# Optimization experiments

Hardware: AMD Instinct MI355X
Metric: run time of the kernel (lower is better)

## Reference

```python
import jax, jax.numpy as jnp
import numpy as np

H, D, G = 8, 64, 64          # num_heads, head_dim, num_slices
HID = H * D                  # 512
EPS = 1e-5
N = 100000


def setup_inputs() -> dict:
    key = jax.random.key(0)
    ks = jax.random.split(key, 16)
    s = 0.02  # init scale
    return {
        "x": jax.random.normal(ks[0], (N, HID), dtype=jnp.float32),
        # x_proj / fx_proj: Linear(HID -> HID) with bias, eqx stores W as (out, in)
        "Wx": jax.random.normal(ks[1], (HID, HID), dtype=jnp.float32) * s,
        "bx": jax.random.normal(ks[2], (HID,), dtype=jnp.float32) * s,
        "Wfx": jax.random.normal(ks[3], (HID, HID), dtype=jnp.float32) * s,
        "bfx": jax.random.normal(ks[4], (HID,), dtype=jnp.float32) * s,
        # slice_proj: Linear(D -> G) with bias
        "Ws": jax.random.normal(ks[5], (G, D), dtype=jnp.float32) * s,
        "bs": jax.random.normal(ks[6], (G,), dtype=jnp.float32) * s,
        # learned temperature, init 0.5, shape (H,1,1)
        "temperature": jnp.ones((H, 1, 1), dtype=jnp.float32) * 0.5,
        # slice MultiheadAttention (num_heads=1, size D): q/k/v/out proj, no biases (eqx defaults)
        "Wq": jax.random.normal(ks[7], (D, D), dtype=jnp.float32) * s,
        "Wk": jax.random.normal(ks[8], (D, D), dtype=jnp.float32) * s,
        "Wv": jax.random.normal(ks[9], (D, D), dtype=jnp.float32) * s,
        "Wo": jax.random.normal(ks[10], (D, D), dtype=jnp.float32) * s,
        # out_proj: Linear(HID -> HID) with bias
        "Wout": jax.random.normal(ks[11], (HID, HID), dtype=jnp.float32) * s,
        "bout": jax.random.normal(ks[12], (HID,), dtype=jnp.float32) * s,
    }


def reference(x, Wx, bx, Wfx, bfx, Ws, bs, temperature, Wq, Wk, Wv, Wo, Wout, bout):
    n = x.shape[0]
    # token projections, split into heads: (H, N, D)
    x_mid = (x @ Wx.T + bx).reshape(n, H, D).transpose(1, 0, 2)
    fx_mid = (x @ Wfx.T + bfx).reshape(n, H, D).transpose(1, 0, 2)

    # slice weights: proj -> temperature-scaled softmax over G  (H, N, G)
    logits = jnp.einsum('hnd,gd->hng', x_mid, Ws) + bs
    w = jax.nn.softmax(logits * temperature, axis=-1)

    # weighted pooling to slice tokens (H, G, D)
    norm = w.sum(axis=1)                                   # (H, G)
    tokens = jnp.einsum('hnd,hng->hgd', fx_mid, w) / (norm[..., None] + EPS)

    # small single-head attention over the G slice tokens, vmapped over H
    q = jnp.einsum('hgd,od->hgo', tokens, Wq)
    k = jnp.einsum('hgd,od->hgo', tokens, Wk)
    v = jnp.einsum('hgd,od->hgo', tokens, Wv)
    attn = jax.nn.softmax(jnp.einsum('hgd,hkd->hgk', q, k) / jnp.sqrt(jnp.float32(D)), axis=-1)
    out_tok = jnp.einsum('hgk,hkd->hgd', attn, v)
    out_tok = jnp.einsum('hgd,od->hgo', out_tok, Wo)

    # deslice: weighted unpooling back to tokens, merge heads, output projection
    out = jnp.einsum('hgd,hng->hnd', out_tok, w)           # (H, N, D)
    out = out.transpose(1, 0, 2).reshape(n, HID)
    return out @ Wout.T + bout
```

## Files before the change

kernel.cpp:

```cpp
#include <hip/hip_runtime.h>
#include <hip/hip_bf16.h>

#define HID 512
#define NH  8
#define DD  64
#define GG  64
#define EPSF 1e-5f

typedef __attribute__((ext_vector_type(8))) short short8;
typedef __attribute__((ext_vector_type(4))) short short4v;
typedef __attribute__((ext_vector_type(4))) float floatx4;

__device__ __forceinline__ short f2bf(float f) {
    union { float f; unsigned u; } v; v.f = f;
    unsigned r = v.u + 0x7fffu + ((v.u >> 16) & 1u);
    return (short)(r >> 16);
}
__device__ __forceinline__ float bf2f(short s) {
    union { unsigned u; float f; } v;
    v.u = ((unsigned)(unsigned short)s) << 16;
    return v.f;
}

#define GLOAD_LDS16(g, l) __builtin_amdgcn_global_load_lds( \
    (const __attribute__((address_space(1))) unsigned int*)(g), \
    (__attribute__((address_space(3))) unsigned int*)(l), 16, 0, 0)

__global__ __launch_bounds__(256)
void cast_kernel(const float* __restrict__ x, short* __restrict__ xb, int n8) {
    int i = blockIdx.x * 256 + threadIdx.x;
    if (i >= n8) return;
    const float4* p = (const float4*)(x + (size_t)i * 8);
    float4 a = p[0], b = p[1];
    short8 v;
    v[0] = f2bf(a.x); v[1] = f2bf(a.y); v[2] = f2bf(a.z); v[3] = f2bf(a.w);
    v[4] = f2bf(b.x); v[5] = f2bf(b.y); v[6] = f2bf(b.z); v[7] = f2bf(b.w);
    *(short8*)(xb + (size_t)i * 8) = v;
}

__global__ void fold1_kernel(const float* __restrict__ Wx, const float* __restrict__ bx,
                             const float* __restrict__ Wfx, const float* __restrict__ bfx,
                             const float* __restrict__ Ws, const float* __restrict__ bs,
                             const float* __restrict__ temp,
                             short* __restrict__ Wcat, float* __restrict__ bias_cat) {
    int idx = blockIdx.x * 256 + threadIdx.x;
    int row = idx >> 9;
    int k = idx & 511;
    float val;
    if (row < 512) {
        val = Wfx[row * 512 + k];
        if (k == 0) bias_cat[row] = bfx[row];
    } else {
        int hg = row - 512;
        int h = hg >> 6, g = hg & 63;
        float t = temp[h];
        float s = 0.f;
        #pragma unroll 8
        for (int d = 0; d < 64; ++d) s += Ws[g * 64 + d] * Wx[(h * 64 + d) * 512 + k];
        val = s * t;
        if (k == 0) {
            float b = 0.f;
            for (int d = 0; d < 64; ++d) b += Ws[g * 64 + d] * bx[h * 64 + d];
            bias_cat[row] = (b + bs[g]) * t;
        }
    }
    Wcat[idx] = f2bf(val);
}

template <bool OUT_F32, bool FUSE_SM>
__global__ __launch_bounds__(256, 4)
void gemm_bt(const short* __restrict__ A, int lda,
             const short* __restrict__ B,
             const float* __restrict__ bias,
             void* __restrict__ Cp, int ldc,
             int M, int K, int clog2, int Rtiles) {
    __shared__ short As[128 * 64];
    __shared__ short Bs[128 * 64];

    const int id = blockIdx.x;
    const int xcd = id & 7;
    const int s = id >> 3;
    const int cblk = s & ((1 << clog2) - 1);
    const int slice = (Rtiles + 7) >> 3;
    const int rt = xcd * slice + (s >> clog2);
    if (rt >= Rtiles) return;

    const int tid = threadIdx.x;
    const int wid = tid >> 6, lane = tid & 63;
    const int col0 = cblk * 128;
    const int row0 = rt * 128;
    const int wm = (wid >> 1) * 64, wn = (wid & 1) * 64;
    const int lr = lane & 15, lq = lane >> 4;

    int st_row[4], st_kc[4];
    #pragma unroll
    for (int it = 0; it < 4; ++it) {
        int c = tid + it * 256;
        st_row[it] = c >> 3;
        st_kc[it] = (c & 7) ^ (st_row[it] & 7);
    }
    const int fx0 = (lq ^ (lr & 7)) * 8;
    const int fx1 = ((4 + lq) ^ (lr & 7)) * 8;

    floatx4 acc[4][4];
    #pragma unroll
    for (int i = 0; i < 4; ++i)
        #pragma unroll
        for (int j = 0; j < 4; ++j) acc[i][j] = (floatx4)(0.f);

    const short* Abase = A + (size_t)row0 * lda;
    const short* Bbase = B + (size_t)col0 * lda;

    for (int k0 = 0; k0 < K; k0 += 64) {
        #pragma unroll
        for (int it = 0; it < 4; ++it) {
            short* ldsA = As + (wid * 64 + it * 256) * 8;
            short* ldsB = Bs + (wid * 64 + it * 256) * 8;
            GLOAD_LDS16(Abase + (size_t)st_row[it] * lda + k0 + st_kc[it] * 8, ldsA);
            GLOAD_LDS16(Bbase + (size_t)st_row[it] * lda + k0 + st_kc[it] * 8, ldsB);
        }
        __syncthreads();

        short8 af[4], bfr[4];
        #pragma unroll
        for (int i = 0; i < 4; ++i) af[i]  = *(const short8*)&As[(wm + i * 16 + lr) * 64 + fx0];
        #pragma unroll
        for (int j = 0; j < 4; ++j) bfr[j] = *(const short8*)&Bs[(wn + j * 16 + lr) * 64 + fx0];
        #pragma unroll
        for (int i = 0; i < 4; ++i)
            #pragma unroll
            for (int j = 0; j < 4; ++j)
                acc[i][j] = __builtin_amdgcn_mfma_f32_16x16x32_bf16(af[i], bfr[j], acc[i][j], 0, 0, 0);
        #pragma unroll
        for (int i = 0; i < 4; ++i) af[i]  = *(const short8*)&As[(wm + i * 16 + lr) * 64 + fx1];
        #pragma unroll
        for (int j = 0; j < 4; ++j) bfr[j] = *(const short8*)&Bs[(wn + j * 16 + lr) * 64 + fx1];
        #pragma unroll
        for (int i = 0; i < 4; ++i)
            #pragma unroll
            for (int j = 0; j < 4; ++j)
                acc[i][j] = __builtin_amdgcn_mfma_f32_16x16x32_bf16(af[i], bfr[j], acc[i][j], 0, 0, 0);
        __syncthreads();
    }

    const bool do_sm = FUSE_SM && (col0 >= 512);
    float bcol[4];
    #pragma unroll
    for (int j = 0; j < 4; ++j) bcol[j] = bias[col0 + wn + j * 16 + lr];

    #pragma unroll
    for (int i = 0; i < 4; ++i) {
        #pragma unroll
        for (int r = 0; r < 4; ++r) {
            int grow = row0 + wm + i * 16 + lq * 4 + r;
            float v[4];
            #pragma unroll
            for (int j = 0; j < 4; ++j) v[j] = acc[i][j][r] + bcol[j];
            if (do_sm) {
                float m = fmaxf(fmaxf(v[0], v[1]), fmaxf(v[2], v[3]));
                #pragma unroll
                for (int off = 1; off < 16; off <<= 1) m = fmaxf(m, __shfl_xor(m, off));
                float sum = 0.f;
                #pragma unroll
                for (int j = 0; j < 4; ++j) { v[j] = __expf(v[j] - m); sum += v[j]; }
                #pragma unroll
                for (int off = 1; off < 16; off <<= 1) sum += __shfl_xor(sum, off);
                float inv = 1.f / sum;
                #pragma unroll
                for (int j = 0; j < 4; ++j) v[j] *= inv;
            }
            if (grow < M) {
                #pragma unroll
                for (int j = 0; j < 4; ++j) {
                    int gcol = col0 + wn + j * 16 + lr;
                    if constexpr (OUT_F32) ((float*)Cp)[(size_t)grow * ldc + gcol] = v[j];
                    else                   ((short*)Cp)[(size_t)grow * ldc + gcol] = f2bf(v[j]);
                }
            }
        }
    }
}

__global__ __launch_bounds__(256)
void pool_mfma(const short* __restrict__ mid, float* __restrict__ tok_raw,
               float* __restrict__ norm, int N, int chunk) {
    const int h = blockIdx.y;
    const int n0 = blockIdx.x * chunk;
    if (n0 >= N) return;
    const int ksteps = (min(chunk, N - n0)) >> 5;

    const int tid = threadIdx.x;
    const int wid = tid >> 6, lane = tid & 63;
    const int lr = lane & 15, lq = lane >> 4;
    const int wg = (wid >> 1) * 32, wd = (wid & 1) * 32;

    __shared__ short wt[32 * 72];
    __shared__ short ft[32 * 72];

    const int sn = tid >> 3;
    const int sc0 = (tid & 7) * 8;
    const int scr = (sc0 + 16 * ((sn >> 3) & 3)) & 63;
    const int st_off = sn * 72 + scr;

    const int ra = ((wg + lr) + 16 * lq) & 63;
    const int rb = ((wd + lr) + 16 * lq) & 63;

    const short* wbase = mid + (size_t)n0 * 1024 + 512 + h * 64;
    const short* fbase = mid + (size_t)n0 * 1024 + h * 64;

    floatx4 acc[2][2];
    #pragma unroll
    for (int i = 0; i < 2; ++i)
        #pragma unroll
        for (int j = 0; j < 2; ++j) acc[i][j] = (floatx4)(0.f);
    floatx4 accn[2];
    accn[0] = (floatx4)(0.f); accn[1] = (floatx4)(0.f);

    short8 ones;
    #pragma unroll
    for (int j = 0; j < 8; ++j) ones[j] = (short)0x3F80;

    for (int ks = 0; ks < ksteps; ++ks) {
        const size_t roff = (size_t)(ks * 32 + sn) * 1024;
        short8 wv = *(const short8*)(wbase + roff + sc0);
        short8 fv = *(const short8*)(fbase + roff + sc0);
        __syncthreads();
        *(short8*)&wt[st_off] = wv;
        *(short8*)&ft[st_off] = fv;
        __syncthreads();

        short8 af[2], bf_[2];
        #pragma unroll
        for (int i = 0; i < 2; ++i) {
            short tmpv[8];
            #pragma unroll
            for (int j = 0; j < 8; ++j)
                tmpv[j] = wt[(lq * 8 + j) * 72 + ((ra + i * 16) & 63)];
            af[i] = *(const short8*)tmpv;
        }
        #pragma unroll
        for (int j2 = 0; j2 < 2; ++j2) {
            short tmpv[8];
            #pragma unroll
            for (int j = 0; j < 8; ++j)
                tmpv[j] = ft[(lq * 8 + j) * 72 + ((rb + j2 * 16) & 63)];
            bf_[j2] = *(const short8*)tmpv;
        }
        #pragma unroll
        for (int i = 0; i < 2; ++i)
            #pragma unroll
            for (int j = 0; j < 2; ++j)
                acc[i][j] = __builtin_amdgcn_mfma_f32_16x16x32_bf16(af[i], bf_[j], acc[i][j], 0, 0, 0);
        if (wd == 0) {
            #pragma unroll
            for (int i = 0; i < 2; ++i)
                accn[i] = __builtin_amdgcn_mfma_f32_16x16x32_bf16(af[i], ones, accn[i], 0, 0, 0);
        }
    }

    #pragma unroll
    for (int i = 0; i < 2; ++i) {
        #pragma unroll
        for (int r = 0; r < 4; ++r) {
            int g = wg + i * 16 + lq * 4 + r;
            #pragma unroll
            for (int j = 0; j < 2; ++j) {
                int d = wd + j * 16 + lr;
                atomicAdd(&tok_raw[(h * 64 + g) * 64 + d], acc[i][j][r]);
            }
        }
    }
    if (wd == 0 && lr == 0) {
        #pragma unroll
        for (int i = 0; i < 2; ++i)
            #pragma unroll
            for (int r = 0; r < 4; ++r)
                atomicAdd(&norm[h * 64 + wg + i * 16 + lq * 4 + r], accn[i][r]);
    }
}

__global__ __launch_bounds__(256)
void attn_kernel(const float* __restrict__ tok_raw, const float* __restrict__ norm,
                 const float* __restrict__ Wq, const float* __restrict__ Wk,
                 const float* __restrict__ Wv, const float* __restrict__ Wo,
                 float* __restrict__ out_tok) {
    const int h = blockIdx.x;
    const int tid = threadIdx.x;
    const int g = tid & 63, part = tid >> 6;
    const int o0 = part * 16;

    __shared__ float tk[64][65];
    __shared__ float qq[64][65];
    __shared__ float kk[64][65];
    __shared__ float vv[64][65];
    __shared__ float pp[64][65];
    __shared__ float od[64][65];

    const float inv = 1.f / (norm[h * 64 + g] + EPSF);
    #pragma unroll
    for (int dd = 0; dd < 16; ++dd) {
        int d = o0 + dd;
        tk[g][d] = tok_raw[(size_t)(h * 64 + g) * 64 + d] * inv;
    }
    __syncthreads();

    float t[64];
    #pragma unroll
    for (int d = 0; d < 64; ++d) t[d] = tk[g][d];
    #pragma unroll
    for (int oo = 0; oo < 16; ++oo) {
        int o = o0 + oo;
        float sq = 0.f, sk = 0.f, sv = 0.f;
        #pragma unroll
        for (int d = 0; d < 64; ++d) {
            float td = t[d];
            sq += td * Wq[o * 64 + d];
            sk += td * Wk[o * 64 + d];
            sv += td * Wv[o * 64 + d];
        }
        qq[g][o] = sq; kk[g][o] = sk; vv[g][o] = sv;
    }
    __syncthreads();

    float q[64];
    #pragma unroll
    for (int o = 0; o < 64; ++o) q[o] = qq[g][o];
    #pragma unroll
    for (int jj = 0; jj < 16; ++jj) {
        int j = o0 + jj;
        float s = 0.f;
        #pragma unroll
        for (int o = 0; o < 64; ++o) s += q[o] * kk[j][o];
        pp[g][j] = s * 0.125f;
    }
    __syncthreads();

    float sr[64];
    float mx = -1e30f;
    #pragma unroll
    for (int j = 0; j < 64; ++j) { sr[j] = pp[g][j]; mx = fmaxf(mx, sr[j]); }
    float sum = 0.f;
    #pragma unroll
    for (int j = 0; j < 64; ++j) { sr[j] = __expf(sr[j] - mx); sum += sr[j]; }
    const float isum = 1.f / sum;

    #pragma unroll
    for (int dd = 0; dd < 16; ++dd) {
        int d = o0 + dd;
        float a = 0.f;
        #pragma unroll
        for (int j = 0; j < 64; ++j) a += sr[j] * vv[j][d];
        od[g][d] = a * isum;
    }
    __syncthreads();

    float ot[64];
    #pragma unroll
    for (int d = 0; d < 64; ++d) ot[d] = od[g][d];
    #pragma unroll
    for (int oo = 0; oo < 16; ++oo) {
        int o = o0 + oo;
        float a = 0.f;
        #pragma unroll
        for (int d = 0; d < 64; ++d) a += ot[d] * Wo[o * 64 + d];
        out_tok[(size_t)(h * 64 + g) * 64 + o] = a;
    }
}

__global__ void fold2_kernel(const float* __restrict__ out_tok,
                             const float* __restrict__ Wout, short* __restrict__ Vbf) {
    int idx = blockIdx.x * 256 + threadIdx.x;
    int o = idx >> 9, hg = idx & 511;
    int h = hg >> 6;
    const float* ot = out_tok + (size_t)hg * 64;
    const float* wo = Wout + (size_t)o * 512 + h * 64;
    float s = 0.f;
    #pragma unroll 8
    for (int d = 0; d < 64; ++d) s += ot[d] * wo[d];
    Vbf[idx] = f2bf(s);
}

extern "C" void kernel_launch(void* const* d_in, const int* in_sizes, int n_in,
                              void* d_out, int out_size, void* d_ws, size_t ws_size,
                              hipStream_t stream) {
    const float* x    = (const float*)d_in[0];
    const float* Wx   = (const float*)d_in[1];
    const float* bx   = (const float*)d_in[2];
    const float* Wfx  = (const float*)d_in[3];
    const float* bfx  = (const float*)d_in[4];
    const float* Ws   = (const float*)d_in[5];
    const float* bs   = (const float*)d_in[6];
    const float* temp = (const float*)d_in[7];
    const float* Wq   = (const float*)d_in[8];
    const float* Wk   = (const float*)d_in[9];
    const float* Wv   = (const float*)d_in[10];
    const float* Wo   = (const float*)d_in[11];
    const float* Wout = (const float*)d_in[12];
    const float* bout = (const float*)d_in[13];

    const int N = in_sizes[0] / HID;

    char* p = (char*)d_ws;
    short* mid = (short*)p;           p += (size_t)N * 1024 * 2;
    short* Wcat = (short*)p;          p += (size_t)1024 * 512 * 2;
    float* bias_cat = (float*)p;      p += 1024 * 4;
    float* tok_raw = (float*)p;       p += (size_t)NH * GG * DD * 4;
    float* norm_ = (float*)p;         p += (size_t)NH * GG * 4;
    float* out_tok = (float*)p;       p += (size_t)NH * GG * DD * 4;
    short* Vbf = (short*)p;           p += (size_t)512 * 512 * 2;
    short* x_bf = (short*)d_out;

    cast_kernel<<<(N * 512 / 8 + 255) / 256, 256, 0, stream>>>(x, x_bf, N * 512 / 8);
    fold1_kernel<<<2048, 256, 0, stream>>>(Wx, bx, Wfx, bfx, Ws, bs, temp, Wcat, bias_cat);

    const int R = (N + 127) / 128;
    const int slice = (R + 7) / 8;

    gemm_bt<false, true><<<8 * slice * 8, 256, 0, stream>>>(
        x_bf, HID, Wcat, bias_cat, (void*)mid, 1024, N, 512, 3, R);

    hipMemsetAsync(tok_raw, 0, (size_t)(NH * GG * DD + NH * GG) * 4, stream);

    const int chunk = 544;
    dim3 g2((N + chunk - 1) / chunk, 8);
    pool_mfma<<<g2, 256, 0, stream>>>(mid, tok_raw, norm_, N, chunk);

    attn_kernel<<<8, 256, 0, stream>>>(tok_raw, norm_, Wq, Wk, Wv, Wo, out_tok);

    fold2_kernel<<<1024, 256, 0, stream>>>(out_tok, Wout, Vbf);

    gemm_bt<true, false><<<8 * slice * 4, 256, 0, stream>>>(
        mid + 512, 1024, Vbf, bout, d_out, HID, N, 512, 2, R);
}
```

Before: 847.5 us.

## Fuse fp32-to-bf16 cast of x into the first projection GEMM

Drops the standalone cast kernel. A new GEMM variant reads fp32 x directly, converts tiles to bf16 in registers and writes them into LDS, while B still streams in through direct global-to-LDS loads. This removes one full-size write and re-read of the bf16 copy of x. In exchange, each column block repeats the conversion, A-tile loads go through registers with a one-step prefetch, and the fp32 A reads are twice as large per tile.

```diff
diff --git a/kernel.cpp b/kernel.cpp
--- a/kernel.cpp
+++ b/kernel.cpp
@@ -8,7 +8,6 @@
 #define EPSF 1e-5f
 
 typedef __attribute__((ext_vector_type(8))) short short8;
-typedef __attribute__((ext_vector_type(4))) short short4v;
 typedef __attribute__((ext_vector_type(4))) float floatx4;
 
 __device__ __forceinline__ short f2bf(float f) {
@@ -16,27 +15,10 @@
     unsigned r = v.u + 0x7fffu + ((v.u >> 16) & 1u);
     return (short)(r >> 16);
 }
-__device__ __forceinline__ float bf2f(short s) {
-    union { unsigned u; float f; } v;
-    v.u = ((unsigned)(unsigned short)s) << 16;
-    return v.f;
-}
 
 #define GLOAD_LDS16(g, l) __builtin_amdgcn_global_load_lds( \
     (const __attribute__((address_space(1))) unsigned int*)(g), \
     (__attribute__((address_space(3))) unsigned int*)(l), 16, 0, 0)
-
-__global__ __launch_bounds__(256)
-void cast_kernel(const float* __restrict__ x, short* __restrict__ xb, int n8) {
-    int i = blockIdx.x * 256 + threadIdx.x;
-    if (i >= n8) return;
-    const float4* p = (const float4*)(x + (size_t)i * 8);
-    float4 a = p[0], b = p[1];
-    short8 v;
-    v[0] = f2bf(a.x); v[1] = f2bf(a.y); v[2] = f2bf(a.z); v[3] = f2bf(a.w);
-    v[4] = f2bf(b.x); v[5] = f2bf(b.y); v[6] = f2bf(b.z); v[7] = f2bf(b.w);
-    *(short8*)(xb + (size_t)i * 8) = v;
-}
 
 __global__ void fold1_kernel(const float* __restrict__ Wx, const float* __restrict__ bx,
                              const float* __restrict__ Wfx, const float* __restrict__ bfx,
@@ -67,6 +49,142 @@
     Wcat[idx] = f2bf(val);
 }
 
+__global__ __launch_bounds__(256, 4)
+void gemm1_fused(const float* __restrict__ X,
+                 const short* __restrict__ B,
+                 const float* __restrict__ bias,
+                 short* __restrict__ Cp,
+                 int M, int clog2, int Rtiles) {
+    const int K = 512, lda = 512, ldc = 1024;
+    __shared__ short As[128 * 64];
+    __shared__ short Bs[128 * 64];
+
+    const int id = blockIdx.x;
+    const int xcd = id & 7;
+    const int s = id >> 3;
+    const int cblk = s & ((1 << clog2) - 1);
+    const int slice = (Rtiles + 7) >> 3;
+    const int rt = xcd * slice + (s >> clog2);
+    if (rt >= Rtiles) return;
+
+    const int tid = threadIdx.x;
+    const int wid = tid >> 6, lane = tid & 63;
+    const int col0 = cblk * 128;
+    const int row0 = rt * 128;
+    const int wm = (wid >> 1) * 64, wn = (wid & 1) * 64;
+    const int lr = lane & 15, lq = lane >> 4;
+
+    int st_row[4], st_kc[4];
+    const float* aptr[4];
+    #pragma unroll
+    for (int it = 0; it < 4; ++it) {
+        int c = tid + it * 256;
+        st_row[it] = c >> 3;
+        st_kc[it] = (c & 7) ^ (st_row[it] & 7);
+        int ar = min(row0 + st_row[it], M - 1);
+        aptr[it] = X + (size_t)ar * lda + st_kc[it] * 8;
+    }
+    const int fx0 = (lq ^ (lr & 7)) * 8;
+    const int fx1 = ((4 + lq) ^ (lr & 7)) * 8;
+
+    floatx4 acc[4][4];
+    #pragma unroll
+    for (int i = 0; i < 4; ++i)
+        #pragma unroll
+        for (int j = 0; j < 4; ++j) acc[i][j] = (floatx4)(0.f);
+
+    const short* Bbase = B + (size_t)col0 * lda;
+
+    float4 fa[4][2];
+    #pragma unroll
+    for (int it = 0; it < 4; ++it) {
+        fa[it][0] = *(const float4*)(aptr[it]);
+        fa[it][1] = *(const float4*)(aptr[it] + 4);
+    }
+
+    for (int k0 = 0; k0 < K; k0 += 64) {
+        #pragma unroll
+        for (int it = 0; it < 4; ++it) {
+            short* ldsB = Bs + (wid * 64 + it * 256) * 8;
+            GLOAD_LDS16(Bbase + (size_t)st_row[it] * lda + k0 + st_kc[it] * 8, ldsB);
+        }
+        #pragma unroll
+        for (int it = 0; it < 4; ++it) {
+            short8 sv;
+            sv[0] = f2bf(fa[it][0].x); sv[1] = f2bf(fa[it][0].y);
+            sv[2] = f2bf(fa[it][0].z); sv[3] = f2bf(fa[it][0].w);
+            sv[4] = f2bf(fa[it][1].x); sv[5] = f2bf(fa[it][1].y);
+            sv[6] = f2bf(fa[it][1].z); sv[7] = f2bf(fa[it][1].w);
+            *(short8*)&As[(size_t)(tid + it * 256) * 8] = sv;
+        }
+        __syncthreads();
+
+        const int kn = (k0 + 64 < K) ? (k0 + 64) : 0;
+        #pragma unroll
+        for (int it = 0; it < 4; ++it) {
+            fa[it][0] = *(const float4*)(aptr[it] + kn);
+            fa[it][1] = *(const float4*)(aptr[it] + kn + 4);
+        }
+
+        short8 af[4], bfr[4];
+        #pragma unroll
+        for (int i = 0; i < 4; ++i) af[i]  = *(const short8*)&As[(wm + i * 16 + lr) * 64 + fx0];
+        #pragma unroll
+        for (int j = 0; j < 4; ++j) bfr[j] = *(const short8*)&Bs[(wn + j * 16 + lr) * 64 + fx0];
+        #pragma unroll
+        for (int i = 0; i < 4; ++i)
+            #pragma unroll
+            for (int j = 0; j < 4; ++j)
+                acc[i][j] = __builtin_amdgcn_mfma_f32_16x16x32_bf16(af[i], bfr[j], acc[i][j], 0, 0, 0);
+        #pragma unroll
+        for (int i = 0; i < 4; ++i) af[i]  = *(const short8*)&As[(wm + i * 16 + lr) * 64 + fx1];
+        #pragma unroll
+        for (int j = 0; j < 4; ++j) bfr[j] = *(const short8*)&Bs[(wn + j * 16 + lr) * 64 + fx1];
+        #pragma unroll
+        for (int i = 0; i < 4; ++i)
+            #pragma unroll
+            for (int j = 0; j < 4; ++j)
+                acc[i][j] = __builtin_amdgcn_mfma_f32_16x16x32_bf16(af[i], bfr[j], acc[i][j], 0, 0, 0);
+        __syncthreads();
+    }
+
+    const bool do_sm = (col0 >= 512);
+    float bcol[4];
+    #pragma unroll
+    for (int j = 0; j < 4; ++j) bcol[j] = bias[col0 + wn + j * 16 + lr];
+
+    #pragma unroll
+    for (int i = 0; i < 4; ++i) {
+        #pragma unroll
+        for (int r = 0; r < 4; ++r) {
+            int grow = row0 + wm + i * 16 + lq * 4 + r;
+            float v[4];
+            #pragma unroll
+            for (int j = 0; j < 4; ++j) v[j] = acc[i][j][r] + bcol[j];
+            if (do_sm) {
+                float m = fmaxf(fmaxf(v[0], v[1]), fmaxf(v[2], v[3]));
+                #pragma unroll
+                for (int off = 1; off < 16; off <<= 1) m = fmaxf(m, __shfl_xor(m, off));
+                float sum = 0.f;
+                #pragma unroll
+                for (int j = 0; j < 4; ++j) { v[j] = __expf(v[j] - m); sum += v[j]; }
+                #pragma unroll
+                for (int off = 1; off < 16; off <<= 1) sum += __shfl_xor(sum, off);
+                float inv = 1.f / sum;
+                #pragma unroll
+                for (int j = 0; j < 4; ++j) v[j] *= inv;
+            }
+            if (grow < M) {
+                #pragma unroll
+                for (int j = 0; j < 4; ++j) {
+                    int gcol = col0 + wn + j * 16 + lr;
+                    Cp[(size_t)grow * ldc + gcol] = f2bf(v[j]);
+                }
+            }
+        }
+    }
+}
+
 template <bool OUT_F32, bool FUSE_SM>
 __global__ __launch_bounds__(256, 4)
 void gemm_bt(const short* __restrict__ A, int lda,
@@ -408,18 +526,15 @@
     float* norm_ = (float*)p;         p += (size_t)NH * GG * 4;
     float* out_tok = (float*)p;       p += (size_t)NH * GG * DD * 4;
     short* Vbf = (short*)p;           p += (size_t)512 * 512 * 2;
-    short* x_bf = (short*)d_out;
-
-    cast_kernel<<<(N * 512 / 8 + 255) / 256, 256, 0, stream>>>(x, x_bf, N * 512 / 8);
+
     fold1_kernel<<<2048, 256, 0, stream>>>(Wx, bx, Wfx, bfx, Ws, bs, temp, Wcat, bias_cat);
+    hipMemsetAsync(tok_raw, 0, (size_t)(NH * GG * DD + NH * GG) * 4, stream);
 
     const int R = (N + 127) / 128;
     const int slice = (R + 7) / 8;
 
-    gemm_bt<false, true><<<8 * slice * 8, 256, 0, stream>>>(
-        x_bf, HID, Wcat, bias_cat, (void*)mid, 1024, N, 512, 3, R);
-
-    hipMemsetAsync(tok_raw, 0, (size_t)(NH * GG * DD + NH * GG) * 4, stream);
+    gemm1_fused<<<8 * slice * 8, 256, 0, stream>>>(
+        x, Wcat, bias_cat, mid, N, 3, R);
 
     const int chunk = 544;
     dim3 g2((N + chunk - 1) / chunk, 8);
```

Result: faster. 738.5 us (-12.9%).
